# Kernel tuning notes

Measured on AMD Instinct MI355X. Metric: run time of the kernel, lower is better.

The kernel has to match this reference:

```python
import jax, jax.numpy as jnp
import numpy as np
from jax import lax

LOKAL_GRUP = 7
TOP_K = 2
EPS = 1e-8
CACHE_BONUS = 0.1


def setup_inputs() -> dict:
    key = jax.random.key(0)
    ks = jax.random.split(key, 6)
    B, S, D, E, H = 2, 2048, 1024, 8, 4096
    return {
        "x": jax.random.normal(ks[0], (B, S, D), jnp.float32),
        "uzman_embeddings": jax.random.normal(ks[1], (E, D), jnp.float32) * 0.01,
        "W1": jax.random.normal(ks[2], (E, D, H), jnp.float32) * 0.02,
        "b1": jax.random.normal(ks[3], (E, H), jnp.float32) * 0.02,
        "W2": jax.random.normal(ks[4], (E, H, D), jnp.float32) * 0.02,
        "b2": jax.random.normal(ks[5], (E, D), jnp.float32) * 0.02,
        "onbellek_durumu": jnp.ones((E,), jnp.float32),
    }


def _route(tokens, uzman_embeddings, onbellek_durumu):
    # tokens: [N, D], uzman_embeddings: [E, D]
    # local group selection: top LOKAL_GRUP experts by raw dot product
    sim = tokens @ uzman_embeddings.T                      # [N, E]
    _, local_idx = lax.top_k(sim, LOKAL_GRUP)              # [N, LG]
    # cosine scores within local group
    t_norm = tokens / (jnp.linalg.norm(tokens, axis=-1, keepdims=True) + EPS)
    e_norm = uzman_embeddings / (jnp.linalg.norm(uzman_embeddings, axis=-1, keepdims=True) + EPS)
    local_embs = e_norm[local_idx]                         # [N, LG, D]
    scores = jnp.einsum("nld,nd->nl", local_embs, t_norm)
    scores = scores + CACHE_BONUS * onbellek_durumu[local_idx]
    top_scores, top_local = lax.top_k(scores, TOP_K)       # [N, K]
    global_idx = jnp.take_along_axis(local_idx, top_local, axis=1)  # [N, K]
    weights = jax.nn.softmax(top_scores, axis=-1)          # [N, K]
    # original computes routing in detached numpy -> no grad through gate
    return global_idx, lax.stop_gradient(weights)


def reference(x, uzman_embeddings, W1, b1, W2, b2, onbellek_durumu):
    B, S, D = x.shape
    tokens = x.reshape(-1, D)                              # [N, D]
    global_idx, weights = _route(tokens, uzman_embeddings, onbellek_durumu)
    # run every expert on every token (dense), then gather the top-k outputs
    h = jnp.einsum("nd,edh->enh", tokens, W1) + b1[:, None, :]   # [E, N, H]
    h = jax.nn.gelu(h, approximate=False)                         # torch nn.GELU exact
    out_all = jnp.einsum("enh,ehd->end", h, W2) + b2[:, None, :]  # [E, N, D]
    N = tokens.shape[0]
    out_sel = out_all[global_idx, jnp.arange(N)[:, None]]         # [N, K, D]
    out = jnp.sum(weights[..., None] * out_sel, axis=1)           # [N, D]
    return out.reshape(B, S, D)
```

## Files before the change

### kernel.cpp

```cpp
#include <hip/hip_runtime.h>
#include <hip/hip_bf16.h>

#define NTOK 4096
#define DDIM 1024
#define HDIM 4096
#define NEXP 8
#define NPAIR (NTOK * 2)
#define BM 128
#define BK 64
#define MAXT 72

typedef __attribute__((ext_vector_type(8))) short bf16x8;
typedef __attribute__((ext_vector_type(4))) float f32x4;

struct Misc {
  float enorm[NEXP];
  int cnt[NEXP];
  int cursor[NEXP];
  int nt;
  int pad;
  int te[MAXT];
  int tp0[MAXT];
  int tp1[MAXT];
  int gidx[NTOK * 2];
  float twt[NTOK * 2];
  int rows[NPAIR];
  float pwt[NPAIR];
};

#define OFF_W1T 0ull
#define OFF_W2T 67108864ull
#define OFF_H 134217728ull
#define OFF_XG 201326592ull
#define OFF_MISC 218103808ull

__device__ __forceinline__ unsigned short f2bf(float f) {
  unsigned int u = __float_as_uint(f);
  u += 0x7fffu + ((u >> 16) & 1u);
  return (unsigned short)(u >> 16);
}

__global__ __launch_bounds__(512) void enorm_k(const float* __restrict__ emb, Misc* mi) {
  int w = threadIdx.x >> 6, l = threadIdx.x & 63;
  const float* r = emb + (size_t)w * DDIM;
  float s = 0.f;
  for (int i = l; i < DDIM; i += 64) {
    float v = r[i];
    s += v * v;
  }
  #pragma unroll
  for (int o = 32; o; o >>= 1) s += __shfl_xor(s, o);
  if (l == 0) mi->enorm[w] = sqrtf(s);
}

__global__ __launch_bounds__(64) void route_k(const float* __restrict__ x,
                                              const float* __restrict__ emb,
                                              const float* __restrict__ cache, Misc* mi) {
  int n = blockIdx.x, l = threadIdx.x;
  const float* xr = x + (size_t)n * DDIM;
  float s[NEXP];
  #pragma unroll
  for (int e = 0; e < NEXP; e++) s[e] = 0.f;
  float nr = 0.f;
  for (int i = l; i < DDIM; i += 64) {
    float xv = xr[i];
    nr += xv * xv;
    #pragma unroll
    for (int e = 0; e < NEXP; e++) s[e] += xv * emb[e * DDIM + i];
  }
  #pragma unroll
  for (int o = 32; o; o >>= 1) {
    nr += __shfl_xor(nr, o);
    #pragma unroll
    for (int e = 0; e < NEXP; e++) s[e] += __shfl_xor(s[e], o);
  }
  if (l == 0) {
    float tn = sqrtf(nr) + 1e-8f;
    int exc = 0;
    float mn = s[0];
    for (int e = 1; e < NEXP; e++)
      if (s[e] <= mn) {
        mn = s[e];
        exc = e;
      }
    float sc[NEXP];
    for (int e = 0; e < NEXP; e++)
      sc[e] = s[e] / (tn * (mi->enorm[e] + 1e-8f)) + 0.1f * cache[e];
    int g0 = -1, g1 = -1;
    for (int e = 0; e < NEXP; e++) {
      if (e == exc) continue;
      if (g0 < 0 || sc[e] > sc[g0] || (sc[e] == sc[g0] && s[e] > s[g0])) g0 = e;
    }
    for (int e = 0; e < NEXP; e++) {
      if (e == exc || e == g0) continue;
      if (g1 < 0 || sc[e] > sc[g1] || (sc[e] == sc[g1] && s[e] > s[g1])) g1 = e;
    }
    float e1 = expf(sc[g1] - sc[g0]);
    float w0 = 1.f / (1.f + e1);
    float w1 = e1 * w0;
    mi->gidx[2 * n] = g0;
    mi->gidx[2 * n + 1] = g1;
    mi->twt[2 * n] = w0;
    mi->twt[2 * n + 1] = w1;
    atomicAdd(mi->cnt + g0, 1);
    atomicAdd(mi->cnt + g1, 1);
  }
}

__global__ void scan_k(Misc* mi) {
  if (threadIdx.x != 0) return;
  int off = 0, t = 0;
  for (int e = 0; e < NEXP; e++) {
    mi->cursor[e] = off;
    int c = mi->cnt[e];
    for (int r = 0; r < c; r += BM) {
      mi->te[t] = e;
      mi->tp0[t] = off + r;
      int hi = (r + BM < c) ? (r + BM) : c;
      mi->tp1[t] = off + hi;
      t++;
    }
    off += c;
  }
  mi->nt = t;
}

__global__ __launch_bounds__(256) void scatter_k(Misc* mi) {
  int n = blockIdx.x * 256 + threadIdx.x;
  if (n >= NTOK) return;
  #pragma unroll
  for (int k = 0; k < 2; k++) {
    int e = mi->gidx[2 * n + k];
    int p = atomicAdd(mi->cursor + e, 1);
    mi->rows[p] = n;
    mi->pwt[p] = mi->twt[2 * n + k];
  }
}

__global__ __launch_bounds__(64) void gather_k(const float* __restrict__ x, const Misc* __restrict__ mi,
                                               unsigned short* __restrict__ xg) {
  int p = blockIdx.x, l = threadIdx.x;
  const float4* src = (const float4*)(x + (size_t)mi->rows[p] * DDIM);
  uint2* dst = (uint2*)(xg + (size_t)p * DDIM);
  #pragma unroll
  for (int j = 0; j < 4; j++) {
    float4 v = src[l + j * 64];
    uint2 o;
    o.x = (unsigned)f2bf(v.x) | ((unsigned)f2bf(v.y) << 16);
    o.y = (unsigned)f2bf(v.z) | ((unsigned)f2bf(v.w) << 16);
    dst[l + j * 64] = o;
  }
}

__global__ __launch_bounds__(256) void wconv_k(const float* __restrict__ in,
                                               unsigned short* __restrict__ out, int R, int C) {
  __shared__ float tile[64][65];
  int e = blockIdx.z;
  size_t base = (size_t)e * R * C;
  int c0 = blockIdx.x * 64, r0 = blockIdx.y * 64;
  int t = threadIdx.x;
  #pragma unroll
  for (int i = 0; i < 16; i++) {
    int idx = i * 256 + t;
    int r = idx >> 6, c = idx & 63;
    tile[r][c] = in[base + (size_t)(r0 + r) * C + (c0 + c)];
  }
  __syncthreads();
  #pragma unroll
  for (int i = 0; i < 16; i++) {
    int idx = i * 256 + t;
    int r = idx >> 6, c = idx & 63;
    out[base + (size_t)(c0 + r) * R + (r0 + c)] = f2bf(tile[c][r]);
  }
}

template <int MODE>
__global__ __launch_bounds__(256) void gemm_k(const unsigned short* __restrict__ A,
                                              const unsigned short* __restrict__ B,
                                              const float* __restrict__ bias,
                                              unsigned short* __restrict__ hout,
                                              float* __restrict__ out,
                                              const Misc* __restrict__ mi, int K, int N) {
  int tb = blockIdx.y;
  if (tb >= mi->nt) return;
  int e = mi->te[tb], p0 = mi->tp0[tb], p1 = mi->tp1[tb];
  int n0 = blockIdx.x * 128;
  __shared__ unsigned short Alds[BM * BK];
  __shared__ unsigned short Blds[BM * BK];
  int t = threadIdx.x, w = t >> 6, l = t & 63;
  int wr = w >> 1, wc = w & 1;
  f32x4 zero = {0.f, 0.f, 0.f, 0.f};
  f32x4 acc[4][4];
  #pragma unroll
  for (int m = 0; m < 4; m++)
    #pragma unroll
    for (int n = 0; n < 4; n++) acc[m][n] = zero;
  const unsigned short* Be = B + (size_t)e * N * K;
  int KT = K >> 6;
  int srow = l >> 3;
  int scol = (l & 7) * 16;
  for (int kt = 0; kt < KT; ++kt) {
    int kb = kt * 128;
    #pragma unroll
    for (int j = 0; j < 4; j++) {
      int chunk = w * 4 + j;
      int arow = p0 + chunk * 8 + srow;
      if (arow >= NPAIR) arow = NPAIR - 1;
      const char* ga = (const char*)A + (size_t)arow * K * 2 + kb + scol;
      __builtin_amdgcn_global_load_lds((const __attribute__((address_space(1))) void*)ga,
                                       (__attribute__((address_space(3))) void*)((char*)Alds + chunk * 1024),
                                       16, 0, 0);
      int brow = n0 + chunk * 8 + srow;
      const char* gb = (const char*)Be + (size_t)brow * K * 2 + kb + scol;
      __builtin_amdgcn_global_load_lds((const __attribute__((address_space(1))) void*)gb,
                                       (__attribute__((address_space(3))) void*)((char*)Blds + chunk * 1024),
                                       16, 0, 0);
    }
    __syncthreads();
    #pragma unroll
    for (int kk = 0; kk < 2; kk++) {
      bf16x8 af[4], bfr[4];
      #pragma unroll
      for (int m = 0; m < 4; m++) {
        int row = wr * 64 + m * 16 + (l & 15);
        af[m] = *(const bf16x8*)((const char*)Alds + row * 128 + kk * 64 + (l >> 4) * 16);
      }
      #pragma unroll
      for (int n = 0; n < 4; n++) {
        int row = wc * 64 + n * 16 + (l & 15);
        bfr[n] = *(const bf16x8*)((const char*)Blds + row * 128 + kk * 64 + (l >> 4) * 16);
      }
      #pragma unroll
      for (int m = 0; m < 4; m++)
        #pragma unroll
        for (int n = 0; n < 4; n++)
          acc[m][n] = __builtin_amdgcn_mfma_f32_16x16x32_bf16(af[m], bfr[n], acc[m][n], 0, 0, 0);
    }
    __syncthreads();
  }
  int cbase = n0 + wc * 64 + (l & 15);
  int rbase = wr * 64 + (l >> 4) * 4;
  float bv[4];
  #pragma unroll
  for (int n = 0; n < 4; n++) bv[n] = bias[e * N + cbase + n * 16];
  #pragma unroll
  for (int m = 0; m < 4; m++) {
    #pragma unroll
    for (int j = 0; j < 4; j++) {
      int pr = p0 + rbase + m * 16 + j;
      if (pr >= p1) continue;
      if (MODE == 0) {
        #pragma unroll
        for (int n = 0; n < 4; n++) {
          float v = acc[m][n][j] + bv[n];
          float g = 0.5f * v * (1.f + erff(v * 0.70710678118654752f));
          hout[(size_t)pr * N + (cbase + n * 16)] = f2bf(g);
        }
      } else {
        float wgt = mi->pwt[pr];
        int tok = mi->rows[pr];
        #pragma unroll
        for (int n = 0; n < 4; n++) {
          float v = acc[m][n][j] + bv[n];
          atomicAdd(out + (size_t)tok * DDIM + (cbase + n * 16), wgt * v);
        }
      }
    }
  }
}

extern "C" void kernel_launch(void* const* d_in, const int* in_sizes, int n_in, void* d_out,
                              int out_size, void* d_ws, size_t ws_size, hipStream_t stream) {
  const float* x = (const float*)d_in[0];
  const float* emb = (const float*)d_in[1];
  const float* W1 = (const float*)d_in[2];
  const float* b1 = (const float*)d_in[3];
  const float* W2 = (const float*)d_in[4];
  const float* b2 = (const float*)d_in[5];
  const float* cache = (const float*)d_in[6];
  float* out = (float*)d_out;
  char* ws = (char*)d_ws;
  unsigned short* W1T = (unsigned short*)(ws + OFF_W1T);
  unsigned short* W2T = (unsigned short*)(ws + OFF_W2T);
  unsigned short* hb = (unsigned short*)(ws + OFF_H);
  unsigned short* xg = (unsigned short*)(ws + OFF_XG);
  Misc* mi = (Misc*)(ws + OFF_MISC);

  hipMemsetAsync(out, 0, (size_t)NTOK * DDIM * sizeof(float), stream);
  hipMemsetAsync(mi, 0, sizeof(Misc), stream);

  enorm_k<<<1, 512, 0, stream>>>(emb, mi);
  route_k<<<NTOK, 64, 0, stream>>>(x, emb, cache, mi);
  scan_k<<<1, 1, 0, stream>>>(mi);
  scatter_k<<<NTOK / 256, 256, 0, stream>>>(mi);
  gather_k<<<NPAIR, 64, 0, stream>>>(x, mi, xg);
  wconv_k<<<dim3(HDIM / 64, DDIM / 64, NEXP), 256, 0, stream>>>(W1, W1T, DDIM, HDIM);
  wconv_k<<<dim3(DDIM / 64, HDIM / 64, NEXP), 256, 0, stream>>>(W2, W2T, HDIM, DDIM);
  gemm_k<0><<<dim3(HDIM / 128, MAXT), 256, 0, stream>>>(xg, W1T, b1, hb, nullptr, mi, DDIM, HDIM);
  gemm_k<1><<<dim3(DDIM / 128, MAXT), 256, 0, stream>>>(hb, W2T, b2, nullptr, out, mi, HDIM, DDIM);
}
```

Baseline: 852.6 us.

## Rewrite expert GEMMs with 256x256 tiles, double-buffered LDS, split-K and combine pass

Replaces the 128x128 grouped GEMM with a 512-thread 256x256-tile kernel. The new kernel uses double-buffered, XOR-swizzled LDS staged through global_load_lds, interleaves loads with MFMA phases using barriers and setprio, and remaps workgroups across XCDs. The second GEMM uses split-K=2 and writes partial sums to a workspace buffer. A new combine kernel adds bias and applies the routing weights per token, which removes the atomicAdd scatter and the output memset. The aim is higher MFMA utilization and less LDS/global traffic per flop; the costs are an extra fp32 partial buffer, an extra kernel, and more wasted work on partially filled 256-row tiles.

```diff
diff --git a/kernel.cpp b/kernel.cpp
--- a/kernel.cpp
+++ b/kernel.cpp
@@ -6,9 +6,8 @@
 #define HDIM 4096
 #define NEXP 8
 #define NPAIR (NTOK * 2)
-#define BM 128
-#define BK 64
-#define MAXT 72
+#define BMT 256
+#define MAXT 40
 
 typedef __attribute__((ext_vector_type(8))) short bf16x8;
 typedef __attribute__((ext_vector_type(4))) float f32x4;
@@ -24,15 +23,17 @@
   int tp1[MAXT];
   int gidx[NTOK * 2];
   float twt[NTOK * 2];
+  int ppos[NTOK * 2];
   int rows[NPAIR];
   float pwt[NPAIR];
 };
 
-#define OFF_W1T 0ull
-#define OFF_W2T 67108864ull
-#define OFF_H 134217728ull
-#define OFF_XG 201326592ull
-#define OFF_MISC 218103808ull
+#define OFF_W2T 0ull
+#define OFF_H 0x4000000ull
+#define OFF_XG 0x8000000ull
+#define OFF_W1T 0x9000000ull
+#define OFF_OUTP 0x8000000ull
+#define OFF_MISC 0xD000000ull
 
 __device__ __forceinline__ unsigned short f2bf(float f) {
   unsigned int u = __float_as_uint(f);
@@ -113,10 +114,10 @@
   for (int e = 0; e < NEXP; e++) {
     mi->cursor[e] = off;
     int c = mi->cnt[e];
-    for (int r = 0; r < c; r += BM) {
+    for (int r = 0; r < c; r += BMT) {
       mi->te[t] = e;
       mi->tp0[t] = off + r;
-      int hi = (r + BM < c) ? (r + BM) : c;
+      int hi = (r + BMT < c) ? (r + BMT) : c;
       mi->tp1[t] = off + hi;
       t++;
     }
@@ -134,6 +135,7 @@
     int p = atomicAdd(mi->cursor + e, 1);
     mi->rows[p] = n;
     mi->pwt[p] = mi->twt[2 * n + k];
+    mi->ppos[2 * n + k] = p;
   }
 }
 
@@ -174,99 +176,222 @@
   }
 }
 
+#define GL(src, off)                                                                        \
+  __builtin_amdgcn_global_load_lds((const __attribute__((address_space(1))) void*)(src),    \
+                                   (__attribute__((address_space(3))) void*)(LDS + (off)),  \
+                                   16, 0, 0)
+
 template <int MODE>
-__global__ __launch_bounds__(256) void gemm_k(const unsigned short* __restrict__ A,
-                                              const unsigned short* __restrict__ B,
-                                              const float* __restrict__ bias,
-                                              unsigned short* __restrict__ hout,
-                                              float* __restrict__ out,
-                                              const Misc* __restrict__ mi, int K, int N) {
-  int tb = blockIdx.y;
+__global__ __launch_bounds__(512, 2) void gemm8_k(const unsigned short* __restrict__ A,
+                                                  const unsigned short* __restrict__ B,
+                                                  const float* __restrict__ bias,
+                                                  unsigned short* __restrict__ hout,
+                                                  float* __restrict__ outp,
+                                                  const Misc* __restrict__ mi, int K, int N,
+                                                  int nk) {
+  __shared__ char LDS[131072];
+  int nwg = gridDim.x * gridDim.y * gridDim.z;
+  int lin = (blockIdx.z * gridDim.y + blockIdx.y) * gridDim.x + blockIdx.x;
+  int q = nwg >> 3, r = nwg & 7, xc = lin & 7;
+  int wk = (xc < r ? xc * (q + 1) : r * (q + 1) + (xc - r) * q) + (lin >> 3);
+  int nb = wk % gridDim.x;
+  int rest = wk / gridDim.x;
+  int tb = rest % gridDim.y;
+  int ks = rest / gridDim.y;
   if (tb >= mi->nt) return;
   int e = mi->te[tb], p0 = mi->tp0[tb], p1 = mi->tp1[tb];
-  int n0 = blockIdx.x * 128;
-  __shared__ unsigned short Alds[BM * BK];
-  __shared__ unsigned short Blds[BM * BK];
-  int t = threadIdx.x, w = t >> 6, l = t & 63;
-  int wr = w >> 1, wc = w & 1;
+  int n0 = nb * 256;
+  int k0 = ks * nk;
+  int tid = threadIdx.x, w = tid >> 6, l = tid & 63;
+  int wr = w >> 2, wc = w & 3;
+  int srow = l >> 3;
+  int scol = ((l & 7) ^ srow) << 4;
+  size_t ldb = (size_t)K * 2;
+  const char* Asrc[4];
+  const char* Bsrc[4];
+  #pragma unroll
+  for (int j = 0; j < 4; j++) {
+    int ar = p0 + j * 64 + w * 8 + srow;
+    if (ar > NPAIR - 1) ar = NPAIR - 1;
+    Asrc[j] = (const char*)A + (size_t)ar * ldb + scol;
+    int br = n0 + j * 64 + w * 8 + srow;
+    Bsrc[j] = (const char*)B + (size_t)e * N * ldb + (size_t)br * ldb + scol;
+  }
+  f32x4 acc[8][4];
   f32x4 zero = {0.f, 0.f, 0.f, 0.f};
-  f32x4 acc[4][4];
-  #pragma unroll
-  for (int m = 0; m < 4; m++)
+  #pragma unroll
+  for (int m = 0; m < 8; m++)
     #pragma unroll
     for (int n = 0; n < 4; n++) acc[m][n] = zero;
-  const unsigned short* Be = B + (size_t)e * N * K;
-  int KT = K >> 6;
-  int srow = l >> 3;
-  int scol = (l & 7) * 16;
-  for (int kt = 0; kt < KT; ++kt) {
-    int kb = kt * 128;
-    #pragma unroll
-    for (int j = 0; j < 4; j++) {
-      int chunk = w * 4 + j;
-      int arow = p0 + chunk * 8 + srow;
-      if (arow >= NPAIR) arow = NPAIR - 1;
-      const char* ga = (const char*)A + (size_t)arow * K * 2 + kb + scol;
-      __builtin_amdgcn_global_load_lds((const __attribute__((address_space(1))) void*)ga,
-                                       (__attribute__((address_space(3))) void*)((char*)Alds + chunk * 1024),
-                                       16, 0, 0);
-      int brow = n0 + chunk * 8 + srow;
-      const char* gb = (const char*)Be + (size_t)brow * K * 2 + kb + scol;
-      __builtin_amdgcn_global_load_lds((const __attribute__((address_space(1))) void*)gb,
-                                       (__attribute__((address_space(3))) void*)((char*)Blds + chunk * 1024),
-                                       16, 0, 0);
-    }
-    __syncthreads();
-    #pragma unroll
-    for (int kk = 0; kk < 2; kk++) {
-      bf16x8 af[4], bfr[4];
-      #pragma unroll
-      for (int m = 0; m < 4; m++) {
-        int row = wr * 64 + m * 16 + (l & 15);
-        af[m] = *(const bf16x8*)((const char*)Alds + row * 128 + kk * 64 + (l >> 4) * 16);
-      }
-      #pragma unroll
-      for (int n = 0; n < 4; n++) {
-        int row = wc * 64 + n * 16 + (l & 15);
-        bfr[n] = *(const bf16x8*)((const char*)Blds + row * 128 + kk * 64 + (l >> 4) * 16);
-      }
-      #pragma unroll
-      for (int m = 0; m < 4; m++)
-        #pragma unroll
-        for (int n = 0; n < 4; n++)
-          acc[m][n] = __builtin_amdgcn_mfma_f32_16x16x32_bf16(af[m], bfr[n], acc[m][n], 0, 0, 0);
-    }
-    __syncthreads();
+  int q4 = l >> 4, s3 = l & 7;
+  int colk0 = ((q4 ^ (s3 & 3)) << 4) | ((s3 >> 2) << 6);
+  int aoffB = (wr * 128 + (l & 15)) * 128 + colk0;
+  int boffB = 32768 + (wc * 64 + (l & 15)) * 128 + colk0;
+
+  long kb0 = (long)k0 * 128;
+  #pragma unroll
+  for (int j = 0; j < 4; j++) GL(Asrc[j] + kb0, j * 8192 + w * 1024);
+  #pragma unroll
+  for (int j = 0; j < 4; j++) GL(Bsrc[j] + kb0, 32768 + j * 8192 + w * 1024);
+  if (nk > 1) {
+    GL(Asrc[0] + kb0 + 128, 65536 + w * 1024);
+    GL(Asrc[1] + kb0 + 128, 65536 + 8192 + w * 1024);
+  }
+
+  bf16x8 af[4][2], bf[4][2];
+  for (int t = 0; t < nk; ++t) {
+    int cb = (t & 1) << 16, nbuf = ((t + 1) & 1) << 16;
+    long kb1 = (long)(k0 + t + 1) * 128;
+    long kb2 = kb1 + 128;
+    int ao = cb + aoffB, bo = cb + boffB;
+    bool ld1 = (t + 1 < nk), ld2 = (t + 2 < nk);
+    if (ld1)
+      asm volatile("s_waitcnt vmcnt(2)" ::: "memory");
+    else
+      asm volatile("s_waitcnt vmcnt(0)" ::: "memory");
+    __builtin_amdgcn_s_barrier();
+    asm volatile("" ::: "memory");
+    if (ld1) {
+      GL(Asrc[2] + kb1, nbuf + 2 * 8192 + w * 1024);
+      GL(Asrc[3] + kb1, nbuf + 3 * 8192 + w * 1024);
+    }
+    #pragma unroll
+    for (int m = 0; m < 4; m++)
+      #pragma unroll
+      for (int kk = 0; kk < 2; kk++)
+        af[m][kk] = *(const bf16x8*)(LDS + ((ao + m * 2048) ^ (kk << 6)));
+    #pragma unroll
+    for (int n = 0; n < 2; n++)
+      #pragma unroll
+      for (int kk = 0; kk < 2; kk++)
+        bf[n][kk] = *(const bf16x8*)(LDS + ((bo + n * 2048) ^ (kk << 6)));
+    asm volatile("s_waitcnt lgkmcnt(0)" ::: "memory");
+    __builtin_amdgcn_sched_barrier(0);
+    __builtin_amdgcn_s_setprio(1);
+    #pragma unroll
+    for (int m = 0; m < 4; m++)
+      #pragma unroll
+      for (int n = 0; n < 2; n++)
+        #pragma unroll
+        for (int kk = 0; kk < 2; kk++)
+          acc[m][n] = __builtin_amdgcn_mfma_f32_16x16x32_bf16(af[m][kk], bf[n][kk], acc[m][n], 0, 0, 0);
+    __builtin_amdgcn_s_setprio(0);
+    __builtin_amdgcn_s_barrier();
+    asm volatile("" ::: "memory");
+    if (ld1) {
+      GL(Bsrc[0] + kb1, nbuf + 32768 + w * 1024);
+      GL(Bsrc[1] + kb1, nbuf + 32768 + 8192 + w * 1024);
+    }
+    #pragma unroll
+    for (int n = 0; n < 2; n++)
+      #pragma unroll
+      for (int kk = 0; kk < 2; kk++)
+        bf[2 + n][kk] = *(const bf16x8*)(LDS + ((bo + (2 + n) * 2048) ^ (kk << 6)));
+    asm volatile("s_waitcnt lgkmcnt(0)" ::: "memory");
+    __builtin_amdgcn_sched_barrier(0);
+    __builtin_amdgcn_s_setprio(1);
+    #pragma unroll
+    for (int m = 0; m < 4; m++)
+      #pragma unroll
+      for (int n = 0; n < 2; n++)
+        #pragma unroll
+        for (int kk = 0; kk < 2; kk++)
+          acc[m][2 + n] = __builtin_amdgcn_mfma_f32_16x16x32_bf16(af[m][kk], bf[2 + n][kk], acc[m][2 + n], 0, 0, 0);
+    __builtin_amdgcn_s_setprio(0);
+    __builtin_amdgcn_s_barrier();
+    asm volatile("" ::: "memory");
+    if (ld1) {
+      GL(Bsrc[2] + kb1, nbuf + 32768 + 2 * 8192 + w * 1024);
+      GL(Bsrc[3] + kb1, nbuf + 32768 + 3 * 8192 + w * 1024);
+    }
+    #pragma unroll
+    for (int m = 0; m < 4; m++)
+      #pragma unroll
+      for (int kk = 0; kk < 2; kk++)
+        af[m][kk] = *(const bf16x8*)(LDS + ((ao + 8192 + m * 2048) ^ (kk << 6)));
+    asm volatile("s_waitcnt lgkmcnt(0)" ::: "memory");
+    __builtin_amdgcn_sched_barrier(0);
+    __builtin_amdgcn_s_setprio(1);
+    #pragma unroll
+    for (int m = 0; m < 4; m++)
+      #pragma unroll
+      for (int n = 0; n < 2; n++)
+        #pragma unroll
+        for (int kk = 0; kk < 2; kk++)
+          acc[4 + m][2 + n] = __builtin_amdgcn_mfma_f32_16x16x32_bf16(af[m][kk], bf[2 + n][kk], acc[4 + m][2 + n], 0, 0, 0);
+    __builtin_amdgcn_s_setprio(0);
+    __builtin_amdgcn_s_barrier();
+    asm volatile("" ::: "memory");
+    if (ld2) {
+      GL(Asrc[0] + kb2, cb + w * 1024);
+      GL(Asrc[1] + kb2, cb + 8192 + w * 1024);
+    }
+    __builtin_amdgcn_s_setprio(1);
+    #pragma unroll
+    for (int m = 0; m < 4; m++)
+      #pragma unroll
+      for (int n = 0; n < 2; n++)
+        #pragma unroll
+        for (int kk = 0; kk < 2; kk++)
+          acc[4 + m][n] = __builtin_amdgcn_mfma_f32_16x16x32_bf16(af[m][kk], bf[n][kk], acc[4 + m][n], 0, 0, 0);
+    __builtin_amdgcn_s_setprio(0);
+    __builtin_amdgcn_s_barrier();
+    asm volatile("" ::: "memory");
   }
   int cbase = n0 + wc * 64 + (l & 15);
-  int rbase = wr * 64 + (l >> 4) * 4;
-  float bv[4];
-  #pragma unroll
-  for (int n = 0; n < 4; n++) bv[n] = bias[e * N + cbase + n * 16];
-  #pragma unroll
-  for (int m = 0; m < 4; m++) {
-    #pragma unroll
-    for (int j = 0; j < 4; j++) {
-      int pr = p0 + rbase + m * 16 + j;
-      if (pr >= p1) continue;
-      if (MODE == 0) {
+  if (MODE == 0) {
+    float bv[4];
+    #pragma unroll
+    for (int n = 0; n < 4; n++) bv[n] = bias[e * N + cbase + n * 16];
+    #pragma unroll
+    for (int m = 0; m < 8; m++) {
+      #pragma unroll
+      for (int jj = 0; jj < 4; jj++) {
+        int pr = p0 + wr * 128 + m * 16 + q4 * 4 + jj;
+        if (pr >= p1) continue;
         #pragma unroll
         for (int n = 0; n < 4; n++) {
-          float v = acc[m][n][j] + bv[n];
+          float v = acc[m][n][jj] + bv[n];
           float g = 0.5f * v * (1.f + erff(v * 0.70710678118654752f));
-          hout[(size_t)pr * N + (cbase + n * 16)] = f2bf(g);
-        }
-      } else {
-        float wgt = mi->pwt[pr];
-        int tok = mi->rows[pr];
-        #pragma unroll
-        for (int n = 0; n < 4; n++) {
-          float v = acc[m][n][j] + bv[n];
-          atomicAdd(out + (size_t)tok * DDIM + (cbase + n * 16), wgt * v);
+          hout[(size_t)pr * N + cbase + n * 16] = f2bf(g);
         }
       }
     }
-  }
+  } else {
+    float* op = outp + (size_t)ks * NPAIR * DDIM;
+    #pragma unroll
+    for (int m = 0; m < 8; m++) {
+      #pragma unroll
+      for (int jj = 0; jj < 4; jj++) {
+        int pr = p0 + wr * 128 + m * 16 + q4 * 4 + jj;
+        if (pr >= p1) continue;
+        #pragma unroll
+        for (int n = 0; n < 4; n++) op[(size_t)pr * N + cbase + n * 16] = acc[m][n][jj];
+      }
+    }
+  }
+}
+
+__global__ __launch_bounds__(256) void combine_k(const float* __restrict__ op,
+                                                 const float* __restrict__ b2,
+                                                 const Misc* __restrict__ mi,
+                                                 float* __restrict__ out) {
+  int tok = blockIdx.x, i = threadIdx.x;
+  int pa = mi->ppos[2 * tok], pb = mi->ppos[2 * tok + 1];
+  float w0 = mi->twt[2 * tok], w1 = mi->twt[2 * tok + 1];
+  int e0 = mi->gidx[2 * tok], e1 = mi->gidx[2 * tok + 1];
+  const float4* o0 = (const float4*)op;
+  const float4* o1 = (const float4*)(op + (size_t)NPAIR * DDIM);
+  float4 r0a = o0[(size_t)pa * 256 + i], r1a = o1[(size_t)pa * 256 + i];
+  float4 r0b = o0[(size_t)pb * 256 + i], r1b = o1[(size_t)pb * 256 + i];
+  float4 va = ((const float4*)(b2 + (size_t)e0 * DDIM))[i];
+  float4 vb = ((const float4*)(b2 + (size_t)e1 * DDIM))[i];
+  float4 res;
+  res.x = w0 * (r0a.x + r1a.x + va.x) + w1 * (r0b.x + r1b.x + vb.x);
+  res.y = w0 * (r0a.y + r1a.y + va.y) + w1 * (r0b.y + r1b.y + vb.y);
+  res.z = w0 * (r0a.z + r1a.z + va.z) + w1 * (r0b.z + r1b.z + vb.z);
+  res.w = w0 * (r0a.w + r1a.w + va.w) + w1 * (r0b.w + r1b.w + vb.w);
+  ((float4*)out)[(size_t)tok * 256 + i] = res;
 }
 
 extern "C" void kernel_launch(void* const* d_in, const int* in_sizes, int n_in, void* d_out,
@@ -284,9 +409,9 @@
   unsigned short* W2T = (unsigned short*)(ws + OFF_W2T);
   unsigned short* hb = (unsigned short*)(ws + OFF_H);
   unsigned short* xg = (unsigned short*)(ws + OFF_XG);
+  float* outp = (float*)(ws + OFF_OUTP);
   Misc* mi = (Misc*)(ws + OFF_MISC);
 
-  hipMemsetAsync(out, 0, (size_t)NTOK * DDIM * sizeof(float), stream);
   hipMemsetAsync(mi, 0, sizeof(Misc), stream);
 
   enorm_k<<<1, 512, 0, stream>>>(emb, mi);
@@ -296,6 +421,7 @@
   gather_k<<<NPAIR, 64, 0, stream>>>(x, mi, xg);
   wconv_k<<<dim3(HDIM / 64, DDIM / 64, NEXP), 256, 0, stream>>>(W1, W1T, DDIM, HDIM);
   wconv_k<<<dim3(DDIM / 64, HDIM / 64, NEXP), 256, 0, stream>>>(W2, W2T, HDIM, DDIM);
-  gemm_k<0><<<dim3(HDIM / 128, MAXT), 256, 0, stream>>>(xg, W1T, b1, hb, nullptr, mi, DDIM, HDIM);
-  gemm_k<1><<<dim3(DDIM / 128, MAXT), 256, 0, stream>>>(hb, W2T, b2, nullptr, out, mi, HDIM, DDIM);
-}
+  gemm8_k<0><<<dim3(HDIM / 256, MAXT, 1), 512, 0, stream>>>(xg, W1T, b1, hb, nullptr, mi, DDIM, HDIM, 16);
+  gemm8_k<1><<<dim3(DDIM / 256, MAXT, 2), 512, 0, stream>>>(hb, W2T, nullptr, nullptr, outp, mi, HDIM, DDIM, 32);
+  combine_k<<<NTOK, 256, 0, stream>>>(outp, b2, mi, out);
+}
```

Result: faster. 747.0 us (-12.4%).
